# Performance work log

Hardware: AMD Instinct MI355X
Metric: run time of the kernel (lower is better)

## Reference

```python
import jax, jax.numpy as jnp
import numpy as np

B, N, D = 4, 2048, 1024
H, HD = 16, 64
MAX_SEQ = 4096
INNER = H * HD


def setup_inputs() -> dict:
    key = jax.random.key(0)
    ks = jax.random.split(key, 5)
    s = 0.02
    return {
        "x": jax.random.normal(ks[0], (B, N, D), dtype=jnp.float32),
        "ln_gamma": jnp.ones((D,), jnp.float32),
        "ln_beta": jnp.zeros((D,), jnp.float32),
        "w_qkv": jax.random.normal(ks[1], (D, 3 * INNER), dtype=jnp.float32) * s,
        "w_out": jax.random.normal(ks[2], (INNER, D), dtype=jnp.float32) * s,
        "b_out": jnp.zeros((D,), jnp.float32),
    }


def _rope_tables(n, head_dim):
    inv_freq = 1.0 / (10000.0 ** (jnp.arange(0, head_dim, 2, dtype=jnp.float32) / head_dim))
    pos = jnp.arange(n, dtype=jnp.float32)
    ang = pos[:, None] * inv_freq[None, :]  # [n, hd/2]
    return jnp.sin(ang), jnp.cos(ang)


def reference(x, ln_gamma, ln_beta, w_qkv, w_out, b_out):
    b, n, d = x.shape
    # LayerNorm
    mu = jnp.mean(x, axis=-1, keepdims=True)
    var = jnp.var(x, axis=-1, keepdims=True)
    xn = (x - mu) / jnp.sqrt(var + 1e-5) * ln_gamma + ln_beta
    # QKV projection (no bias)
    qkv = xn @ w_qkv  # [b, n, 3*inner]
    q, k, v = jnp.split(qkv, 3, axis=-1)
    def to_heads(t):
        return t.reshape(b, n, H, HD).transpose(0, 2, 1, 3)  # b h n d
    q, k, v = to_heads(q), to_heads(k), to_heads(v)
    # RoPE (half-split rotation, as in source)
    sin, cos = _rope_tables(n, HD)  # [n, hd/2]
    sin = sin[None, None]
    cos = cos[None, None]
    half = HD // 2
    def rotate(t):
        t1, t2 = t[..., :half], t[..., half:]
        return jnp.concatenate([t1 * cos - t2 * sin, t2 * cos + t1 * sin], axis=-1)
    qr, kr = rotate(q), rotate(k)
    scale = HD ** -0.5
    scores = jnp.einsum('bhid,bhjd->bhij', qr, kr) * scale
    probs = jax.nn.softmax(scores, axis=-1)
    out = jnp.einsum('bhij,bhjd->bhid', probs, v)
    out = out.transpose(0, 2, 1, 3).reshape(b, n, INNER)
    return out @ w_out + b_out
```

## Files before the change

kernel.cpp:

```cpp
#include <hip/hip_runtime.h>
#include <hip/hip_bf16.h>

#define Bb   4
#define Nn   2048
#define Dd   1024
#define Hh   16
#define HDd  64
#define IN3  3072
#define RR   8192

typedef __attribute__((ext_vector_type(8))) short short8;
typedef __attribute__((ext_vector_type(4))) float floatx4;

#define MFMA16(a, b, c) __builtin_amdgcn_mfma_f32_16x16x32_bf16((a), (b), (c), 0, 0, 0)

static __device__ __forceinline__ unsigned short f2bf(float f) {
    union { float f; unsigned int u; } v; v.f = f;
    unsigned int r = v.u + 0x7fffu + ((v.u >> 16) & 1u);
    return (unsigned short)(r >> 16);
}
static __device__ __forceinline__ float bf2f(unsigned short h) {
    union { unsigned int u; float f; } v; v.u = ((unsigned int)h) << 16;
    return v.f;
}

static __device__ __forceinline__ float fast_exp2(float x) {
#if __has_builtin(__builtin_amdgcn_exp2f)
    return __builtin_amdgcn_exp2f(x);
#else
    return exp2f(x);
#endif
}

typedef const __attribute__((address_space(1))) void* gas1_t;
typedef __attribute__((address_space(3))) void* las3_t;
static __device__ __forceinline__ void load_lds16(const void* g, void* l) {
    __builtin_amdgcn_global_load_lds((gas1_t)(unsigned long long)g,
                                     (las3_t)(unsigned int)(unsigned long long)l,
                                     16, 0, 0);
}

__global__ void transpose_w(const float* __restrict__ src, unsigned short* __restrict__ dst,
                            int rows, int cols) {
    __shared__ float tile[32][33];
    int c0 = blockIdx.x * 32, r0 = blockIdx.y * 32;
    int tx = threadIdx.x, ty = threadIdx.y;
#pragma unroll
    for (int i = 0; i < 4; ++i) tile[ty + 8 * i][tx] = src[(r0 + ty + 8 * i) * cols + c0 + tx];
    __syncthreads();
#pragma unroll
    for (int i = 0; i < 4; ++i) dst[(c0 + ty + 8 * i) * rows + r0 + tx] = f2bf(tile[tx][ty + 8 * i]);
}

__global__ __launch_bounds__(256) void ln_kernel(const float* __restrict__ x,
                                                 const float* __restrict__ g,
                                                 const float* __restrict__ be,
                                                 unsigned short* __restrict__ xn) {
    int row = blockIdx.x, t = threadIdx.x;
    float4 v = ((const float4*)(x + row * Dd))[t];
    float s  = v.x + v.y + v.z + v.w;
    float sq = v.x * v.x + v.y * v.y + v.z * v.z + v.w * v.w;
#pragma unroll
    for (int off = 1; off < 64; off <<= 1) { s += __shfl_xor(s, off); sq += __shfl_xor(sq, off); }
    __shared__ float ps[4], pq2[4];
    int wv = t >> 6;
    if ((t & 63) == 0) { ps[wv] = s; pq2[wv] = sq; }
    __syncthreads();
    s  = ps[0] + ps[1] + ps[2] + ps[3];
    sq = pq2[0] + pq2[1] + pq2[2] + pq2[3];
    float mu   = s * (1.0f / Dd);
    float var  = sq * (1.0f / Dd) - mu * mu;
    float rstd = rsqrtf(var + 1e-5f);
    float4 gg = ((const float4*)g)[t];
    float4 bb = ((const float4*)be)[t];
    ushort4 o;
    o.x = f2bf((v.x - mu) * rstd * gg.x + bb.x);
    o.y = f2bf((v.y - mu) * rstd * gg.y + bb.y);
    o.z = f2bf((v.z - mu) * rstd * gg.z + bb.z);
    o.w = f2bf((v.w - mu) * rstd * gg.w + bb.w);
    ((ushort4*)(xn + row * Dd))[t] = o;
}

__global__ __launch_bounds__(256) void gemm_qkv(const unsigned short* __restrict__ A,
                                                const unsigned short* __restrict__ Bt,
                                                unsigned short* __restrict__ qo,
                                                unsigned short* __restrict__ ko,
                                                unsigned short* __restrict__ vo) {
    __shared__ unsigned short As[128 * 64];
    __shared__ unsigned short Bs[128 * 64];
    int r0 = blockIdx.x * 128, c0 = blockIdx.y * 128;
    int tid = threadIdx.x;
    int wave = tid >> 6, lane = tid & 63, l15 = lane & 15, quad = lane >> 4;
    int wm = wave & 1, wn = wave >> 1;
    floatx4 acc[4][4] = {};
    int srow8 = lane >> 3;
    int scol  = (lane & 7) * 8;
    for (int k0 = 0; k0 < 1024; k0 += 64) {
#pragma unroll
        for (int i = 0; i < 4; ++i) {
            int row = (wave * 4 + i) * 8 + srow8;
            load_lds16(&A[(r0 + row) * 1024 + k0 + scol],  &As[row * 64 + scol]);
            load_lds16(&Bt[(c0 + row) * 1024 + k0 + scol], &Bs[row * 64 + scol]);
        }
        __syncthreads();
#pragma unroll
        for (int ks = 0; ks < 2; ++ks) {
            short8 af[4], bf[4];
#pragma unroll
            for (int mi = 0; mi < 4; ++mi)
                af[mi] = *(const short8*)&As[(wm * 64 + mi * 16 + l15) * 64 + ks * 32 + quad * 8];
#pragma unroll
            for (int ni = 0; ni < 4; ++ni)
                bf[ni] = *(const short8*)&Bs[(wn * 64 + ni * 16 + l15) * 64 + ks * 32 + quad * 8];
#pragma unroll
            for (int mi = 0; mi < 4; ++mi)
#pragma unroll
                for (int ni = 0; ni < 4; ++ni)
                    acc[mi][ni] = MFMA16(af[mi], bf[ni], acc[mi][ni]);
        }
        __syncthreads();
    }
    unsigned short* outp = (c0 < 1024) ? qo : (c0 < 2048) ? ko : vo;
#pragma unroll
    for (int ni = 0; ni < 4; ++ni) {
        int c = c0 + wn * 64 + ni * 16 + l15;
        int cin = c & 1023;
        int h = cin >> 6, j = cin & 63;
#pragma unroll
        for (int mi = 0; mi < 4; ++mi) {
#pragma unroll
            for (int r2 = 0; r2 < 4; ++r2) {
                int rr = r0 + wm * 64 + mi * 16 + quad * 4 + r2;
                int b = rr >> 11, n = rr & 2047;
                int bh = b * 16 + h;
                outp[(bh * 2048 + n) * 64 + j] = f2bf(acc[mi][ni][r2]);
            }
        }
    }
}

__global__ __launch_bounds__(256) void vtrans(const unsigned short* __restrict__ v,
                                              unsigned short* __restrict__ vt) {
    __shared__ unsigned short T[64][72];
    int bh = blockIdx.y, n0 = blockIdx.x * 64;
    int t = threadIdx.x;
    int nl = t >> 2, c = (t & 3) * 16;
    const unsigned short* src = v + ((bh * 2048) + n0 + nl) * 64 + c;
    *(short8*)&T[nl][c]     = *(const short8*)src;
    *(short8*)&T[nl][c + 8] = *(const short8*)(src + 8);
    __syncthreads();
    int hd = t >> 2, nc = (t & 3) * 16;
    unsigned short tmp[16];
#pragma unroll
    for (int i = 0; i < 16; ++i) {
        int pos = nc + i;
        int blk = pos >> 5, p = pos & 31;
        int kq = (p >> 3) & 3, hh = (p >> 2) & 1, r = p & 3;
        tmp[i] = T[blk * 32 + hh * 16 + kq * 4 + r][hd];
    }
    unsigned short* dst = vt + ((bh * 64) + hd) * 2048 + n0 + nc;
    *(short8*)dst       = *(const short8*)&tmp[0];
    *(short8*)(dst + 8) = *(const short8*)&tmp[8];
}

__global__ __launch_bounds__(256) void rope_kernel(unsigned short* __restrict__ q,
                                                   unsigned short* __restrict__ k) {
    int idx = blockIdx.x * 256 + threadIdx.x;
    int j  = idx & 31;
    int n  = (idx >> 5) & 2047;
    int bh = idx >> 16;
    int base = (bh * 2048 + n) * 64;
    float inv = exp2f(-(float)j * (13.287712379549449f / 32.0f));
    float ang = (float)n * inv;
    float sa = sinf(ang), ca = cosf(ang);
    float q1 = bf2f(q[base + j]), q2 = bf2f(q[base + j + 32]);
    q[base + j]      = f2bf(q1 * ca - q2 * sa);
    q[base + j + 32] = f2bf(q2 * ca + q1 * sa);
    float k1 = bf2f(k[base + j]), k2 = bf2f(k[base + j + 32]);
    k[base + j]      = f2bf(k1 * ca - k2 * sa);
    k[base + j + 32] = f2bf(k2 * ca + k1 * sa);
}

__global__ __launch_bounds__(256, 4) void attn_kernel(const unsigned short* __restrict__ q,
                                                      const unsigned short* __restrict__ k,
                                                      const unsigned short* __restrict__ vt,
                                                      unsigned short* __restrict__ attn) {
    __shared__ unsigned short KVs[2][2][64 * 64];
    int bh = blockIdx.y, q0 = blockIdx.x * 128;
    int tid = threadIdx.x;
    int wave = tid >> 6, lane = tid & 63, l15 = lane & 15, quad = lane >> 4;
    const unsigned short* qb  = q  + bh * (Nn * HDd);
    const unsigned short* kbp = k  + bh * (Nn * HDd);
    const unsigned short* vb  = vt + bh * (HDd * Nn);
    int qbase = q0 + wave * 32;

    short8 bq[2][2];
#pragma unroll
    for (int g = 0; g < 2; ++g) {
        bq[g][0] = *(const short8*)&qb[(qbase + g * 16 + l15) * 64 + quad * 8];
        bq[g][1] = *(const short8*)&qb[(qbase + g * 16 + l15) * 64 + 32 + quad * 8];
    }

    auto stage = [&](int buf, int kb0) {
#pragma unroll
        for (int i = 0; i < 2; ++i) {
            int c = wave * 2 + i;
            int p = c * 64 + lane;
            int row = p >> 3, pr = p & 7;
            int sc = pr ^ (row & 7);
            load_lds16(&kbp[(kb0 + row) * 64 + sc * 8], &KVs[buf][0][p * 8]);
            load_lds16(&vb[row * Nn + kb0 + sc * 8],    &KVs[buf][1][p * 8]);
        }
    };

    floatx4 ot[2][4] = {};
    float l_run[2] = {0.0f, 0.0f};
    const float sc2 = 0.125f * 1.4426950408889634f;
    int swz0 = (quad ^ (l15 & 7)) << 3;
    int swz1 = ((4 | quad) ^ (l15 & 7)) << 3;

    auto body = [&](int cur, int kt) {
        if (kt < 31) stage(cur ^ 1, (kt + 1) * 64);
        const unsigned short* Kc = KVs[cur][0];
        const unsigned short* Vc = KVs[cur][1];
        short8 ka0[4], ka1[4];
#pragma unroll
        for (int mb = 0; mb < 4; ++mb) {
            ka0[mb] = *(const short8*)&Kc[(mb * 16 + l15) * 64 + swz0];
            ka1[mb] = *(const short8*)&Kc[(mb * 16 + l15) * 64 + swz1];
        }
        floatx4 st[2][4];
#pragma unroll
        for (int g = 0; g < 2; ++g)
#pragma unroll
            for (int mb = 0; mb < 4; ++mb) {
                floatx4 z = {0.0f, 0.0f, 0.0f, 0.0f};
                z = MFMA16(ka0[mb], bq[g][0], z);
                st[g][mb] = MFMA16(ka1[mb], bq[g][1], z);
            }
        short8 pa[2][2];
#pragma unroll
        for (int g = 0; g < 2; ++g) {
            float sump = 0.0f;
#pragma unroll
            for (int c = 0; c < 2; ++c) {
                union { ushort4 u[2]; short8 s; } w;
#pragma unroll
                for (int t2 = 0; t2 < 2; ++t2) {
                    int mb = 2 * c + t2;
                    float p0 = fast_exp2(st[g][mb][0] * sc2);
                    float p1 = fast_exp2(st[g][mb][1] * sc2);
                    float p2 = fast_exp2(st[g][mb][2] * sc2);
                    float p3 = fast_exp2(st[g][mb][3] * sc2);
                    sump += (p0 + p1) + (p2 + p3);
                    *(__hip_bfloat162*)&w.u[t2].x = __float22bfloat162_rn(float2{p0, p1});
                    *(__hip_bfloat162*)&w.u[t2].z = __float22bfloat162_rn(float2{p2, p3});
                }
                pa[g][c] = w.s;
            }
            l_run[g] += sump;
        }
#pragma unroll
        for (int ht = 0; ht < 4; ++ht) {
            int row = (ht * 16 + l15) * 64;
            short8 bv0 = *(const short8*)&Vc[row + swz0];
            short8 bv1 = *(const short8*)&Vc[row + swz1];
#pragma unroll
            for (int g = 0; g < 2; ++g) {
                ot[g][ht] = MFMA16(pa[g][0], bv0, ot[g][ht]);
                ot[g][ht] = MFMA16(pa[g][1], bv1, ot[g][ht]);
            }
        }
        __syncthreads();
    };

    stage(0, 0);
    __syncthreads();
    for (int kt = 0; kt < 32; kt += 2) {
        body(0, kt);
        body(1, kt + 1);
    }
    float il[2][4];
#pragma unroll
    for (int g = 0; g < 2; ++g) {
        float l = l_run[g];
        l += __shfl_xor(l, 16);
        l += __shfl_xor(l, 32);
        float invl = 1.0f / l;
#pragma unroll
        for (int r = 0; r < 4; ++r) il[g][r] = __shfl(invl, quad * 4 + r);
    }
    unsigned short* ob = ((unsigned short*)KVs) + wave * 4096;
#pragma unroll
    for (int g = 0; g < 2; ++g)
#pragma unroll
        for (int ht = 0; ht < 4; ++ht)
#pragma unroll
            for (int r = 0; r < 4; ++r)
                ob[(g * 16 + quad * 4 + r) * 72 + ht * 16 + l15] = f2bf(ot[g][ht][r] * il[g][r]);
    int b = bh >> 4, h = bh & 15;
#pragma unroll
    for (int pass = 0; pass < 2; ++pass) {
        int q_loc = pass * 16 + (lane >> 2), seg = lane & 3;
        unsigned short* dst = attn + ((long)(b * Nn + q0 + wave * 32 + q_loc)) * 1024 + h * 64 + seg * 16;
        *(short8*)dst       = *(const short8*)&ob[q_loc * 72 + seg * 16];
        *(short8*)(dst + 8) = *(const short8*)&ob[q_loc * 72 + seg * 16 + 8];
    }
}

__global__ __launch_bounds__(256) void gemm_out(const unsigned short* __restrict__ A,
                                                const unsigned short* __restrict__ Bt,
                                                const float* __restrict__ bout,
                                                float* __restrict__ out) {
    __shared__ unsigned short As[128 * 64];
    __shared__ unsigned short Bs[128 * 64];
    int r0 = blockIdx.x * 128, c0 = blockIdx.y * 128;
    int tid = threadIdx.x;
    int wave = tid >> 6, lane = tid & 63, l15 = lane & 15, quad = lane >> 4;
    int wm = wave & 1, wn = wave >> 1;
    floatx4 acc[4][4] = {};
    int srow8 = lane >> 3;
    int scol  = (lane & 7) * 8;
    for (int k0 = 0; k0 < 1024; k0 += 64) {
#pragma unroll
        for (int i = 0; i < 4; ++i) {
            int row = (wave * 4 + i) * 8 + srow8;
            load_lds16(&A[(r0 + row) * 1024 + k0 + scol],  &As[row * 64 + scol]);
            load_lds16(&Bt[(c0 + row) * 1024 + k0 + scol], &Bs[row * 64 + scol]);
        }
        __syncthreads();
#pragma unroll
        for (int ks = 0; ks < 2; ++ks) {
            short8 af[4], bf[4];
#pragma unroll
            for (int mi = 0; mi < 4; ++mi)
                af[mi] = *(const short8*)&As[(wm * 64 + mi * 16 + l15) * 64 + ks * 32 + quad * 8];
#pragma unroll
            for (int ni = 0; ni < 4; ++ni)
                bf[ni] = *(const short8*)&Bs[(wn * 64 + ni * 16 + l15) * 64 + ks * 32 + quad * 8];
#pragma unroll
            for (int mi = 0; mi < 4; ++mi)
#pragma unroll
                for (int ni = 0; ni < 4; ++ni)
                    acc[mi][ni] = MFMA16(af[mi], bf[ni], acc[mi][ni]);
        }
        __syncthreads();
    }
#pragma unroll
    for (int ni = 0; ni < 4; ++ni) {
        int c = c0 + wn * 64 + ni * 16 + l15;
        float bias = bout[c];
#pragma unroll
        for (int mi = 0; mi < 4; ++mi)
#pragma unroll
            for (int r2 = 0; r2 < 4; ++r2) {
                int rr = r0 + wm * 64 + mi * 16 + quad * 4 + r2;
                out[rr * 1024 + c] = acc[mi][ni][r2] + bias;
            }
    }
}

extern "C" void kernel_launch(void* const* d_in, const int* in_sizes, int n_in,
                              void* d_out, int out_size, void* d_ws, size_t ws_size,
                              hipStream_t stream) {
    const float* x    = (const float*)d_in[0];
    const float* g    = (const float*)d_in[1];
    const float* be   = (const float*)d_in[2];
    const float* wqkv = (const float*)d_in[3];
    const float* wout = (const float*)d_in[4];
    const float* bout = (const float*)d_in[5];
    float* out = (float*)d_out;

    char* ws = (char*)d_ws;
    unsigned short* xn    = (unsigned short*)(ws);
    unsigned short* wqkvT = (unsigned short*)(ws + 16777216);
    unsigned short* woutT = (unsigned short*)(ws + 23068672);
    unsigned short* qb    = (unsigned short*)(ws + 25165824);
    unsigned short* kb    = (unsigned short*)(ws + 41943040);
    unsigned short* vt    = (unsigned short*)(ws + 58720256);
    unsigned short* attn  = (unsigned short*)(ws + 75497472);
    unsigned short* vtmp  = attn;

    transpose_w<<<dim3(IN3 / 32, Dd / 32), dim3(32, 8), 0, stream>>>(wqkv, wqkvT, Dd, IN3);
    transpose_w<<<dim3(Dd / 32, Dd / 32), dim3(32, 8), 0, stream>>>(wout, woutT, Dd, Dd);
    ln_kernel<<<RR, 256, 0, stream>>>(x, g, be, xn);
    gemm_qkv<<<dim3(RR / 128, IN3 / 128), 256, 0, stream>>>(xn, wqkvT, qb, kb, vtmp);
    vtrans<<<dim3(Nn / 64, Bb * Hh), 256, 0, stream>>>(vtmp, vt);
    rope_kernel<<<(64 * 2048 * 32) / 256, 256, 0, stream>>>(qb, kb);
    attn_kernel<<<dim3(Nn / 128, Bb * Hh), 256, 0, stream>>>(qb, kb, vt, attn);
    gemm_out<<<dim3(RR / 128, Dd / 128), 256, 0, stream>>>(attn, woutT, bout, out);
}
```

Baseline: 301.3 us.

## Fuse RoPE into QKV GEMM epilogue and widen attention query tile

The standalone RoPE kernel is removed. The rotation is now applied to the Q and K accumulators in the QKV GEMM epilogue, using hardware sin/cos on angles reduced to revolutions, which saves a full read and write of Q and K in bf16. The attention kernel now handles 256 queries per block (64 per wave) instead of 128, so each staged K/V tile is reused across twice as many queries. V fragments are loaded once per tile and the per-group epilogue writes through a smaller LDS scratch. The cost is more registers per wave, a launch bound of 2 blocks instead of 4, and half as many attention blocks, which may reduce latency hiding.

```diff
diff --git a/kernel.cpp b/kernel.cpp
--- a/kernel.cpp
+++ b/kernel.cpp
@@ -29,6 +29,18 @@
     return __builtin_amdgcn_exp2f(x);
 #else
     return exp2f(x);
+#endif
+}
+
+static __device__ __forceinline__ void sincos_rev(float ang, float& s, float& c) {
+#if __has_builtin(__builtin_amdgcn_sinf) && __has_builtin(__builtin_amdgcn_cosf)
+    float rev = ang * 0.15915494309189535f;
+    rev = rev - floorf(rev);
+    s = __builtin_amdgcn_sinf(rev);
+    c = __builtin_amdgcn_cosf(rev);
+#else
+    s = sinf(ang);
+    c = cosf(ang);
 #endif
 }
 
@@ -120,6 +132,27 @@
         }
         __syncthreads();
     }
+    if (c0 < 2048) {
+        const float crope = 13.287712379549449f / 32.0f;
+        float invf0 = fast_exp2(-(float)l15 * crope);
+        float invf1 = fast_exp2(-(float)(l15 + 16) * crope);
+#pragma unroll
+        for (int mi = 0; mi < 4; ++mi)
+#pragma unroll
+            for (int r2 = 0; r2 < 4; ++r2) {
+                int rr = r0 + wm * 64 + mi * 16 + quad * 4 + r2;
+                float n = (float)(rr & 2047);
+                float s0, c0r, s1, c1r;
+                sincos_rev(n * invf0, s0, c0r);
+                sincos_rev(n * invf1, s1, c1r);
+                float t1a = acc[mi][0][r2], t2a = acc[mi][2][r2];
+                acc[mi][0][r2] = t1a * c0r - t2a * s0;
+                acc[mi][2][r2] = t2a * c0r + t1a * s0;
+                float t1b = acc[mi][1][r2], t2b = acc[mi][3][r2];
+                acc[mi][1][r2] = t1b * c1r - t2b * s1;
+                acc[mi][3][r2] = t2b * c1r + t1b * s1;
+            }
+    }
     unsigned short* outp = (c0 < 1024) ? qo : (c0 < 2048) ? ko : vo;
 #pragma unroll
     for (int ni = 0; ni < 4; ++ni) {
@@ -163,40 +196,22 @@
     *(short8*)(dst + 8) = *(const short8*)&tmp[8];
 }
 
-__global__ __launch_bounds__(256) void rope_kernel(unsigned short* __restrict__ q,
-                                                   unsigned short* __restrict__ k) {
-    int idx = blockIdx.x * 256 + threadIdx.x;
-    int j  = idx & 31;
-    int n  = (idx >> 5) & 2047;
-    int bh = idx >> 16;
-    int base = (bh * 2048 + n) * 64;
-    float inv = exp2f(-(float)j * (13.287712379549449f / 32.0f));
-    float ang = (float)n * inv;
-    float sa = sinf(ang), ca = cosf(ang);
-    float q1 = bf2f(q[base + j]), q2 = bf2f(q[base + j + 32]);
-    q[base + j]      = f2bf(q1 * ca - q2 * sa);
-    q[base + j + 32] = f2bf(q2 * ca + q1 * sa);
-    float k1 = bf2f(k[base + j]), k2 = bf2f(k[base + j + 32]);
-    k[base + j]      = f2bf(k1 * ca - k2 * sa);
-    k[base + j + 32] = f2bf(k2 * ca + k1 * sa);
-}
-
-__global__ __launch_bounds__(256, 4) void attn_kernel(const unsigned short* __restrict__ q,
+__global__ __launch_bounds__(256, 2) void attn_kernel(const unsigned short* __restrict__ q,
                                                       const unsigned short* __restrict__ k,
                                                       const unsigned short* __restrict__ vt,
                                                       unsigned short* __restrict__ attn) {
     __shared__ unsigned short KVs[2][2][64 * 64];
-    int bh = blockIdx.y, q0 = blockIdx.x * 128;
+    int bh = blockIdx.y, q0 = blockIdx.x * 256;
     int tid = threadIdx.x;
     int wave = tid >> 6, lane = tid & 63, l15 = lane & 15, quad = lane >> 4;
     const unsigned short* qb  = q  + bh * (Nn * HDd);
     const unsigned short* kbp = k  + bh * (Nn * HDd);
     const unsigned short* vb  = vt + bh * (HDd * Nn);
-    int qbase = q0 + wave * 32;
-
-    short8 bq[2][2];
-#pragma unroll
-    for (int g = 0; g < 2; ++g) {
+    int qbase = q0 + wave * 64;
+
+    short8 bq[4][2];
+#pragma unroll
+    for (int g = 0; g < 4; ++g) {
         bq[g][0] = *(const short8*)&qb[(qbase + g * 16 + l15) * 64 + quad * 8];
         bq[g][1] = *(const short8*)&qb[(qbase + g * 16 + l15) * 64 + 32 + quad * 8];
     }
@@ -213,8 +228,8 @@
         }
     };
 
-    floatx4 ot[2][4] = {};
-    float l_run[2] = {0.0f, 0.0f};
+    floatx4 ot[4][4] = {};
+    float l_run[4] = {0.0f, 0.0f, 0.0f, 0.0f};
     const float sc2 = 0.125f * 1.4426950408889634f;
     int swz0 = (quad ^ (l15 & 7)) << 3;
     int swz1 = ((4 | quad) ^ (l15 & 7)) << 3;
@@ -229,18 +244,23 @@
             ka0[mb] = *(const short8*)&Kc[(mb * 16 + l15) * 64 + swz0];
             ka1[mb] = *(const short8*)&Kc[(mb * 16 + l15) * 64 + swz1];
         }
-        floatx4 st[2][4];
-#pragma unroll
-        for (int g = 0; g < 2; ++g)
+        short8 bv0[4], bv1[4];
+#pragma unroll
+        for (int ht = 0; ht < 4; ++ht) {
+            int row = (ht * 16 + l15) * 64;
+            bv0[ht] = *(const short8*)&Vc[row + swz0];
+            bv1[ht] = *(const short8*)&Vc[row + swz1];
+        }
+#pragma unroll
+        for (int g = 0; g < 4; ++g) {
+            floatx4 st[4];
 #pragma unroll
             for (int mb = 0; mb < 4; ++mb) {
                 floatx4 z = {0.0f, 0.0f, 0.0f, 0.0f};
                 z = MFMA16(ka0[mb], bq[g][0], z);
-                st[g][mb] = MFMA16(ka1[mb], bq[g][1], z);
-            }
-        short8 pa[2][2];
-#pragma unroll
-        for (int g = 0; g < 2; ++g) {
+                st[mb] = MFMA16(ka1[mb], bq[g][1], z);
+            }
+            short8 pa[2];
             float sump = 0.0f;
 #pragma unroll
             for (int c = 0; c < 2; ++c) {
@@ -248,27 +268,21 @@
 #pragma unroll
                 for (int t2 = 0; t2 < 2; ++t2) {
                     int mb = 2 * c + t2;
-                    float p0 = fast_exp2(st[g][mb][0] * sc2);
-                    float p1 = fast_exp2(st[g][mb][1] * sc2);
-                    float p2 = fast_exp2(st[g][mb][2] * sc2);
-                    float p3 = fast_exp2(st[g][mb][3] * sc2);
+                    float p0 = fast_exp2(st[mb][0] * sc2);
+                    float p1 = fast_exp2(st[mb][1] * sc2);
+                    float p2 = fast_exp2(st[mb][2] * sc2);
+                    float p3 = fast_exp2(st[mb][3] * sc2);
                     sump += (p0 + p1) + (p2 + p3);
                     *(__hip_bfloat162*)&w.u[t2].x = __float22bfloat162_rn(float2{p0, p1});
                     *(__hip_bfloat162*)&w.u[t2].z = __float22bfloat162_rn(float2{p2, p3});
                 }
-                pa[g][c] = w.s;
+                pa[c] = w.s;
             }
             l_run[g] += sump;
-        }
-#pragma unroll
-        for (int ht = 0; ht < 4; ++ht) {
-            int row = (ht * 16 + l15) * 64;
-            short8 bv0 = *(const short8*)&Vc[row + swz0];
-            short8 bv1 = *(const short8*)&Vc[row + swz1];
-#pragma unroll
-            for (int g = 0; g < 2; ++g) {
-                ot[g][ht] = MFMA16(pa[g][0], bv0, ot[g][ht]);
-                ot[g][ht] = MFMA16(pa[g][1], bv1, ot[g][ht]);
+#pragma unroll
+            for (int ht = 0; ht < 4; ++ht) {
+                ot[g][ht] = MFMA16(pa[0], bv0[ht], ot[g][ht]);
+                ot[g][ht] = MFMA16(pa[1], bv1[ht], ot[g][ht]);
             }
         }
         __syncthreads();
@@ -280,29 +294,24 @@
         body(0, kt);
         body(1, kt + 1);
     }
-    float il[2][4];
-#pragma unroll
-    for (int g = 0; g < 2; ++g) {
+    int b = bh >> 4, h = bh & 15;
+    unsigned short* ob = ((unsigned short*)KVs) + wave * 1152;
+#pragma unroll
+    for (int g = 0; g < 4; ++g) {
         float l = l_run[g];
         l += __shfl_xor(l, 16);
         l += __shfl_xor(l, 32);
         float invl = 1.0f / l;
-#pragma unroll
-        for (int r = 0; r < 4; ++r) il[g][r] = __shfl(invl, quad * 4 + r);
-    }
-    unsigned short* ob = ((unsigned short*)KVs) + wave * 4096;
-#pragma unroll
-    for (int g = 0; g < 2; ++g)
+        float il[4];
+#pragma unroll
+        for (int r = 0; r < 4; ++r) il[r] = __shfl(invl, quad * 4 + r);
 #pragma unroll
         for (int ht = 0; ht < 4; ++ht)
 #pragma unroll
             for (int r = 0; r < 4; ++r)
-                ob[(g * 16 + quad * 4 + r) * 72 + ht * 16 + l15] = f2bf(ot[g][ht][r] * il[g][r]);
-    int b = bh >> 4, h = bh & 15;
-#pragma unroll
-    for (int pass = 0; pass < 2; ++pass) {
-        int q_loc = pass * 16 + (lane >> 2), seg = lane & 3;
-        unsigned short* dst = attn + ((long)(b * Nn + q0 + wave * 32 + q_loc)) * 1024 + h * 64 + seg * 16;
+                ob[(quad * 4 + r) * 72 + ht * 16 + l15] = f2bf(ot[g][ht][r] * il[r]);
+        int q_loc = lane >> 2, seg = lane & 3;
+        unsigned short* dst = attn + ((long)(b * Nn + q0 + wave * 64 + g * 16 + q_loc)) * 1024 + h * 64 + seg * 16;
         *(short8*)dst       = *(const short8*)&ob[q_loc * 72 + seg * 16];
         *(short8*)(dst + 8) = *(const short8*)&ob[q_loc * 72 + seg * 16 + 8];
     }
@@ -386,7 +395,6 @@
     ln_kernel<<<RR, 256, 0, stream>>>(x, g, be, xn);
     gemm_qkv<<<dim3(RR / 128, IN3 / 128), 256, 0, stream>>>(xn, wqkvT, qb, kb, vtmp);
     vtrans<<<dim3(Nn / 64, Bb * Hh), 256, 0, stream>>>(vtmp, vt);
-    rope_kernel<<<(64 * 2048 * 32) / 256, 256, 0, stream>>>(qb, kb);
-    attn_kernel<<<dim3(Nn / 128, Bb * Hh), 256, 0, stream>>>(qb, kb, vt, attn);
+    attn_kernel<<<dim3(Nn / 256, Bb * Hh), 256, 0, stream>>>(qb, kb, vt, attn);
     gemm_out<<<dim3(RR / 128, Dd / 128), 256, 0, stream>>>(attn, woutT, bout, out);
 }
```

New measurement: 290.4 us. -3.6%, faster.
